# Optimization experiments

Measured on AMD Instinct MI355X. Metric: run time of the kernel, lower is better.

The kernel has to match this reference:

```python
import jax, jax.numpy as jnp
import numpy as np

DIM = 1024
DIM_HEAD = 64
HEADS = 8
MULT = 4
ATTN_INNER = HEADS * DIM_HEAD            # 512
FF_INNER = MULT * DIM                    # 4096
FUSED = ATTN_INNER + DIM_HEAD + DIM_HEAD + 2 * FF_INNER  # 8832


def setup_inputs() -> dict:
    key = jax.random.key(0)
    ks = jax.random.split(key, 5)
    x = jax.random.normal(ks[0], (2, 2048, DIM), dtype=jnp.float32)
    gamma = jnp.ones((DIM,), dtype=jnp.float32)
    # Linear weights stored as [in, out]
    w_fused = jax.random.normal(ks[1], (DIM, FUSED), dtype=jnp.float32) * (DIM ** -0.5)
    w_attn_out = jax.random.normal(ks[2], (ATTN_INNER, DIM), dtype=jnp.float32) * (ATTN_INNER ** -0.5)
    w_ff_out = jax.random.normal(ks[3], (FF_INNER, DIM), dtype=jnp.float32) * (FF_INNER ** -0.5)
    return {"x": x, "gamma": gamma, "w_fused": w_fused,
            "w_attn_out": w_attn_out, "w_ff_out": w_ff_out}


def _forward(x, gamma, w_fused, w_attn_out, w_ff_out):
    b, n, d = x.shape
    # LayerNorm (beta buffer is zeros)
    mu = jnp.mean(x, axis=-1, keepdims=True)
    var = jnp.mean(jnp.square(x - mu), axis=-1, keepdims=True)
    xn = (x - mu) * jax.lax.rsqrt(var + 1e-5) * gamma
    # fused QKV + FF projection
    proj = jnp.einsum('bnd,df->bnf', xn, w_fused)
    q = proj[..., :ATTN_INNER]
    k = proj[..., ATTN_INNER:ATTN_INNER + DIM_HEAD]
    v = proj[..., ATTN_INNER + DIM_HEAD:ATTN_INNER + 2 * DIM_HEAD]
    ff = proj[..., ATTN_INNER + 2 * DIM_HEAD:]
    # multi-query attention: single shared K/V head of width DIM_HEAD
    q = q.reshape(b, n, HEADS, DIM_HEAD).transpose(0, 2, 1, 3) * (DIM_HEAD ** -0.5)
    sim = jnp.einsum('bhid,bjd->bhij', q, k)
    attn = jax.nn.softmax(sim, axis=-1)
    out = jnp.einsum('bhij,bjd->bhid', attn, v)
    out = out.transpose(0, 2, 1, 3).reshape(b, n, ATTN_INNER)
    attn_out = jnp.einsum('bna,ad->bnd', out, w_attn_out)
    # parallel SwiGLU FF: chunk -> (x_part, gate); silu(gate)*x_part
    ff_x, gate = ff[..., :FF_INNER], ff[..., FF_INNER:]
    ff_out = jnp.einsum('bnf,fd->bnd', jax.nn.silu(gate) * ff_x, w_ff_out)
    return attn_out + ff_out


def reference(x, gamma, w_fused, w_attn_out, w_ff_out):
    return _forward(x, gamma, w_fused, w_attn_out, w_ff_out)
```

## Files before the change

### kernel.cpp

```cpp
#include <hip/hip_runtime.h>
#include <hip/hip_bf16.h>
#include <stdint.h>

#define DIM     1024
#define SEQ     2048
#define NTOK    4096
#define HEADS   8
#define DH      64
#define AINNER  512
#define FFI     4096
#define FUSED   8832
#define HCOLS   4608

typedef __attribute__((ext_vector_type(8))) short short8;
typedef __attribute__((ext_vector_type(4))) short short4v;
typedef __attribute__((ext_vector_type(4))) float f32x4;

__device__ __forceinline__ short f2bf(float f) {
  union { float f; uint32_t u; } v; v.f = f;
  uint32_t r = v.u + 0x7fffu + ((v.u >> 16) & 1u);
  return (short)(r >> 16);
}
__device__ __forceinline__ float bf2f(short s) {
  union { uint32_t u; float f; } v; v.u = ((uint32_t)(uint16_t)s) << 16;
  return v.f;
}
__device__ __forceinline__ void g2l16(const void* g, void* l) {
  __builtin_amdgcn_global_load_lds((const __attribute__((address_space(1))) void*)g,
                                   (__attribute__((address_space(3))) void*)l, 16, 0, 0);
}

#define PH_W4 asm volatile("s_waitcnt vmcnt(4)\ns_barrier" ::: "memory")
#define PH_W2 asm volatile("s_waitcnt vmcnt(2)\ns_barrier" ::: "memory")
#define PH_W0 asm volatile("s_waitcnt vmcnt(0)\ns_barrier" ::: "memory")
#define PH_B  asm volatile("s_barrier" ::: "memory")

__global__ __launch_bounds__(256) void k_prep(const float* __restrict__ wf,
                                              const float* __restrict__ wao,
                                              const float* __restrict__ wfo,
                                              const float* __restrict__ x,
                                              const float* __restrict__ gamma,
                                              short* __restrict__ WtF,
                                              short* __restrict__ Wt2,
                                              short* __restrict__ xn) {
  __shared__ short tile[32][33];
  __shared__ float red[8];
  int bid = blockIdx.x;
  if (bid < 8832) {
    int bx = bid % 276, by = bid / 276;
    int c0 = bx * 32, r0 = by * 32;
    int tx = threadIdx.x & 31, ty = threadIdx.x >> 5;
#pragma unroll
    for (int i = 0; i < 32; i += 8)
      tile[ty + i][tx] = f2bf(wf[(size_t)(r0 + ty + i) * FUSED + c0 + tx]);
    __syncthreads();
#pragma unroll
    for (int i = 0; i < 32; i += 8)
      WtF[(size_t)(c0 + ty + i) * DIM + r0 + tx] = tile[tx][ty + i];
  } else if (bid < 13440) {
    int idx = bid - 8832;
    int bx = idx & 31, by = idx >> 5;
    int c0 = bx * 32, r0 = by * 32;
    int tx = threadIdx.x & 31, ty = threadIdx.x >> 5;
#pragma unroll
    for (int i = 0; i < 32; i += 8) {
      int r = r0 + ty + i;
      float v = (r < AINNER) ? wao[(size_t)r * DIM + c0 + tx]
                             : wfo[(size_t)(r - AINNER) * DIM + c0 + tx];
      tile[ty + i][tx] = f2bf(v);
    }
    __syncthreads();
#pragma unroll
    for (int i = 0; i < 32; i += 8)
      Wt2[(size_t)(c0 + ty + i) * HCOLS + r0 + tx] = tile[tx][ty + i];
  } else {
    int row = bid - 13440;
    int t = threadIdx.x;
    const float4* xr = (const float4*)(x + (size_t)row * DIM);
    float4 v = xr[t];
    float s = v.x + v.y + v.z + v.w;
    float s2 = v.x * v.x + v.y * v.y + v.z * v.z + v.w * v.w;
#pragma unroll
    for (int m = 1; m < 64; m <<= 1) { s += __shfl_xor(s, m); s2 += __shfl_xor(s2, m); }
    int w = t >> 6;
    if ((t & 63) == 0) { red[w] = s; red[4 + w] = s2; }
    __syncthreads();
    s = red[0] + red[1] + red[2] + red[3];
    s2 = red[4] + red[5] + red[6] + red[7];
    float mu = s * (1.f / DIM);
    float rs = rsqrtf(s2 * (1.f / DIM) - mu * mu + 1e-5f);
    const float4* g4 = (const float4*)gamma;
    float4 g = g4[t];
    short4v o;
    o.x = f2bf((v.x - mu) * rs * g.x);
    o.y = f2bf((v.y - mu) * rs * g.y);
    o.z = f2bf((v.z - mu) * rs * g.z);
    o.w = f2bf((v.w - mu) * rs * g.w);
    ((short4v*)(xn + (size_t)row * DIM))[t] = o;
  }
}

__global__ __launch_bounds__(512, 2) void p1(const short* __restrict__ A,
                                             const short* __restrict__ Bt,
                                             short* __restrict__ qb,
                                             short* __restrict__ kbf,
                                             short* __restrict__ vtb,
                                             short* __restrict__ H) {
  extern __shared__ __align__(16) short S[];
  int tid = threadIdx.x, l = tid & 63, w = tid >> 6;
  int hw = blockIdx.y * 37 + blockIdx.x;
  int tile = (hw & 7) * 74 + (hw >> 3);
  int c = tile / 74, j = tile % 74;
  bool fused = j < 64;
  int bx, by;
  if (fused) { int f = c * 64 + j; by = f >> 5; bx = f & 31; }
  else       { int q = c * 10 + (j - 64); by = q / 5; bx = 32 + q % 5; }
  int mBase = by * 256;
  int b0row = fused ? (640 + bx * 128) : ((bx - 32) * 128);
  int b1row = 4736 + bx * 128;

  int srow = w * 8 + (l >> 3);
  int cs = (l & 7) ^ (l >> 3);
  const short* Ag = A + (size_t)(mBase + srow) * DIM + cs * 8;
  const short* Bg0 = Bt + (size_t)(b0row + srow) * DIM + cs * 8;
  const short* Bg1 = Bt + (size_t)(b1row + srow) * DIM + cs * 8;
  int dsto = w * 512 + l * 8;

#define STG_A0(kt, db) { _Pragma("unroll") for (int i = 0; i < 2; ++i) \
    g2l16(Ag + (size_t)(i * 64) * DIM + (kt) * 64, S + (db) * 16384 + i * 4096 + dsto); }
#define STG_A1(kt, db) { _Pragma("unroll") for (int i = 2; i < 4; ++i) \
    g2l16(Ag + (size_t)(i * 64) * DIM + (kt) * 64, S + (db) * 16384 + i * 4096 + dsto); }
#define STG_B0(kt, db) { _Pragma("unroll") for (int i = 0; i < 2; ++i) \
    g2l16(Bg0 + (size_t)(i * 64) * DIM + (kt) * 64, S + 32768 + (db) * 16384 + i * 4096 + dsto); }
#define STG_B1(kt, db) { _Pragma("unroll") for (int i = 0; i < 2; ++i) \
    g2l16(Bg1 + (size_t)(i * 64) * DIM + (kt) * 64, S + 32768 + (db) * 16384 + 8192 + i * 4096 + dsto); }

  const int NT = DIM / 64;
  int c0 = l & 15, kg = l >> 4, cx = l & 7;
  int ch0 = (kg ^ cx) * 8, ch1 = ((4 + kg) ^ cx) * 8;
  int r0 = (l >> 4) * 4;
  f32x4 zero = {0.f, 0.f, 0.f, 0.f};

  if (!fused) {
    STG_A0(0, 0); STG_A1(0, 0); STG_B0(0, 0);
    int wm = w >> 2, wn = w & 3;
    f32x4 acc[8][2];
#pragma unroll
    for (int m = 0; m < 8; ++m) { acc[m][0] = zero; acc[m][1] = zero; }
    for (int kt = 0; kt < NT; ++kt) {
      int db = kt & 1, dbn = db ^ 1;
      PH_W0;
      if (kt + 1 < NT) { STG_A0(kt + 1, dbn); STG_A1(kt + 1, dbn); STG_B0(kt + 1, dbn); }
      const short* Ab = S + db * 16384;
      const short* Bb = S + 32768 + db * 16384;
#pragma unroll
      for (int kkh = 0; kkh < 2; ++kkh) {
        int ch8 = kkh ? ch1 : ch0;
        short8 b0 = *(const short8*)(Bb + (wn * 32 + c0) * 64 + ch8);
        short8 b1 = *(const short8*)(Bb + (wn * 32 + 16 + c0) * 64 + ch8);
        __builtin_amdgcn_s_setprio(1);
#pragma unroll
        for (int m = 0; m < 8; ++m) {
          short8 a = *(const short8*)(Ab + (wm * 128 + m * 16 + c0) * 64 + ch8);
          acc[m][0] = __builtin_amdgcn_mfma_f32_16x16x32_bf16(a, b0, acc[m][0], 0, 0, 0);
          acc[m][1] = __builtin_amdgcn_mfma_f32_16x16x32_bf16(a, b1, acc[m][1], 0, 0, 0);
        }
        __builtin_amdgcn_s_setprio(0);
      }
    }
#pragma unroll
    for (int m = 0; m < 8; ++m)
#pragma unroll
      for (int n = 0; n < 2; ++n)
#pragma unroll
        for (int r = 0; r < 4; ++r) {
          float val = acc[m][n][r];
          int row = mBase + wm * 128 + m * 16 + r0 + r;
          int col = (bx - 32) * 128 + wn * 32 + n * 16 + c0;
          if (col < AINNER)
            qb[(size_t)row * AINNER + col] = f2bf(val);
          else if (col < AINNER + DH)
            kbf[(size_t)row * DH + (col - AINNER)] = f2bf(val);
          else
            vtb[((size_t)(row >> 11) * DH + (col - AINNER - DH)) * SEQ +
                (row & (SEQ - 1))] = f2bf(val);
        }
    return;
  }

  STG_A0(0, 0); STG_B0(0, 0); STG_B1(0, 0); STG_A1(0, 0);
  int ra = (w >> 2) * 64, rb = (w & 3) * 32;
  f32x4 acc[2][2][4][2];
#pragma unroll
  for (int a = 0; a < 2; ++a)
#pragma unroll
    for (int b = 0; b < 2; ++b)
#pragma unroll
      for (int m = 0; m < 4; ++m)
#pragma unroll
        for (int n = 0; n < 2; ++n) acc[a][b][m][n] = zero;

  for (int kt = 0; kt < NT; ++kt) {
    int db = kt & 1, dbn = db ^ 1;
    bool st = kt + 1 < NT;
    const short* Ab = S + db * 16384;
    const short* Bb = S + 32768 + db * 16384;
    short8 a1[4][2], a2[4][2], bF[2][2], bG[2][2];
    PH_W4;
#pragma unroll
    for (int m = 0; m < 4; ++m) {
      a1[m][0] = *(const short8*)(Ab + (ra + m * 16 + c0) * 64 + ch0);
      a1[m][1] = *(const short8*)(Ab + (ra + m * 16 + c0) * 64 + ch1);
    }
#pragma unroll
    for (int n = 0; n < 2; ++n) {
      bF[n][0] = *(const short8*)(Bb + (rb + n * 16 + c0) * 64 + ch0);
      bF[n][1] = *(const short8*)(Bb + (rb + n * 16 + c0) * 64 + ch1);
    }
    if (st) STG_A0(kt + 1, dbn);
    PH_B;
    __builtin_amdgcn_s_setprio(1);
#pragma unroll
    for (int m = 0; m < 4; ++m)
#pragma unroll
      for (int n = 0; n < 2; ++n) {
        acc[0][0][m][n] = __builtin_amdgcn_mfma_f32_16x16x32_bf16(a1[m][0], bF[n][0], acc[0][0][m][n], 0, 0, 0);
        acc[0][0][m][n] = __builtin_amdgcn_mfma_f32_16x16x32_bf16(a1[m][1], bF[n][1], acc[0][0][m][n], 0, 0, 0);
      }
    __builtin_amdgcn_s_setprio(0);
    if (st) PH_W4; else PH_W2;
#pragma unroll
    for (int n = 0; n < 2; ++n) {
      bG[n][0] = *(const short8*)(Bb + 8192 + (rb + n * 16 + c0) * 64 + ch0);
      bG[n][1] = *(const short8*)(Bb + 8192 + (rb + n * 16 + c0) * 64 + ch1);
    }
    if (st) STG_B0(kt + 1, dbn);
    PH_B;
    __builtin_amdgcn_s_setprio(1);
#pragma unroll
    for (int m = 0; m < 4; ++m)
#pragma unroll
      for (int n = 0; n < 2; ++n) {
        acc[0][1][m][n] = __builtin_amdgcn_mfma_f32_16x16x32_bf16(a1[m][0], bG[n][0], acc[0][1][m][n], 0, 0, 0);
        acc[0][1][m][n] = __builtin_amdgcn_mfma_f32_16x16x32_bf16(a1[m][1], bG[n][1], acc[0][1][m][n], 0, 0, 0);
      }
    __builtin_amdgcn_s_setprio(0);
    if (st) PH_W4; else PH_W0;
#pragma unroll
    for (int m = 0; m < 4; ++m) {
      a2[m][0] = *(const short8*)(Ab + 8192 + (ra + m * 16 + c0) * 64 + ch0);
      a2[m][1] = *(const short8*)(Ab + 8192 + (ra + m * 16 + c0) * 64 + ch1);
    }
    if (st) STG_B1(kt + 1, dbn);
    PH_B;
    __builtin_amdgcn_s_setprio(1);
#pragma unroll
    for (int m = 0; m < 4; ++m)
#pragma unroll
      for (int n = 0; n < 2; ++n) {
        acc[1][1][m][n] = __builtin_amdgcn_mfma_f32_16x16x32_bf16(a2[m][0], bG[n][0], acc[1][1][m][n], 0, 0, 0);
        acc[1][1][m][n] = __builtin_amdgcn_mfma_f32_16x16x32_bf16(a2[m][1], bG[n][1], acc[1][1][m][n], 0, 0, 0);
      }
    __builtin_amdgcn_s_setprio(0);
    if (st) STG_A1(kt + 1, dbn);
    __builtin_amdgcn_s_setprio(1);
#pragma unroll
    for (int m = 0; m < 4; ++m)
#pragma unroll
      for (int n = 0; n < 2; ++n) {
        acc[1][0][m][n] = __builtin_amdgcn_mfma_f32_16x16x32_bf16(a2[m][0], bF[n][0], acc[1][0][m][n], 0, 0, 0);
        acc[1][0][m][n] = __builtin_amdgcn_mfma_f32_16x16x32_bf16(a2[m][1], bF[n][1], acc[1][0][m][n], 0, 0, 0);
      }
    __builtin_amdgcn_s_setprio(0);
  }
#undef STG_A0
#undef STG_A1
#undef STG_B0
#undef STG_B1

#pragma unroll
  for (int a = 0; a < 2; ++a)
#pragma unroll
    for (int m = 0; m < 4; ++m)
#pragma unroll
      for (int n = 0; n < 2; ++n)
#pragma unroll
        for (int r = 0; r < 4; ++r) {
          int row = mBase + a * 128 + ra + m * 16 + r0 + r;
          int col = bx * 128 + rb + n * 16 + c0;
          float g = acc[a][1][m][n][r];
          float sg = g / (1.f + __expf(-g));
          H[(size_t)row * HCOLS + AINNER + col] = f2bf(sg * acc[a][0][m][n][r]);
        }
}

__global__ __launch_bounds__(512, 2) void gemm_s(const short* __restrict__ A,
                                                 const short* __restrict__ Bt,
                                                 short* __restrict__ part) {
  extern __shared__ __align__(16) short S[];
  int tid = threadIdx.x, l = tid & 63, w = tid >> 6;
  int hw = (blockIdx.z * 16 + blockIdx.y) * 4 + blockIdx.x;
  int tile = (hw & 7) * 32 + (hw >> 3);
  int bx = tile & 3, by = (tile >> 2) & 15, bz = tile >> 6;
  int mBase = by * 256, nBase = bx * 256;
  int kOff = bz * 1152;

  int srow = w * 8 + (l >> 3);
  int cs = (l & 7) ^ (l >> 3);
  const short* Ag = A + (size_t)(mBase + srow) * HCOLS + kOff + cs * 8;
  const short* Bg = Bt + (size_t)(nBase + srow) * HCOLS + kOff + cs * 8;
  int dsto = w * 512 + l * 8;

#define SG_A0(kt, db) { _Pragma("unroll") for (int i = 0; i < 2; ++i) \
    g2l16(Ag + (size_t)(i * 64) * HCOLS + (kt) * 64, S + (db) * 16384 + i * 4096 + dsto); }
#define SG_A1(kt, db) { _Pragma("unroll") for (int i = 2; i < 4; ++i) \
    g2l16(Ag + (size_t)(i * 64) * HCOLS + (kt) * 64, S + (db) * 16384 + i * 4096 + dsto); }
#define SG_B0(kt, db) { _Pragma("unroll") for (int i = 0; i < 2; ++i) \
    g2l16(Bg + (size_t)(i * 64) * HCOLS + (kt) * 64, S + 32768 + (db) * 16384 + i * 4096 + dsto); }
#define SG_B1(kt, db) { _Pragma("unroll") for (int i = 2; i < 4; ++i) \
    g2l16(Bg + (size_t)(i * 64) * HCOLS + (kt) * 64, S + 32768 + (db) * 16384 + i * 4096 + dsto); }

  const int NT = 18;
  SG_A0(0, 0); SG_B0(0, 0); SG_B1(0, 0); SG_A1(0, 0);

  int c0 = l & 15, kg = l >> 4, cx = l & 7;
  int ch0 = (kg ^ cx) * 8, ch1 = ((4 + kg) ^ cx) * 8;
  int ra = (w >> 2) * 64, rb = (w & 3) * 32;
  f32x4 zero = {0.f, 0.f, 0.f, 0.f};
  f32x4 acc[2][2][4][2];
#pragma unroll
  for (int a = 0; a < 2; ++a)
#pragma unroll
    for (int b = 0; b < 2; ++b)
#pragma unroll
      for (int m = 0; m < 4; ++m)
#pragma unroll
        for (int n = 0; n < 2; ++n) acc[a][b][m][n] = zero;

  for (int kt = 0; kt < NT; ++kt) {
    int db = kt & 1, dbn = db ^ 1;
    bool st = kt + 1 < NT;
    const short* Ab = S + db * 16384;
    const short* Bb = S + 32768 + db * 16384;
    short8 a1[4][2], a2[4][2], bF[2][2], bG[2][2];
    PH_W4;
#pragma unroll
    for (int m = 0; m < 4; ++m) {
      a1[m][0] = *(const short8*)(Ab + (ra + m * 16 + c0) * 64 + ch0);
      a1[m][1] = *(const short8*)(Ab + (ra + m * 16 + c0) * 64 + ch1);
    }
#pragma unroll
    for (int n = 0; n < 2; ++n) {
      bF[n][0] = *(const short8*)(Bb + (rb + n * 16 + c0) * 64 + ch0);
      bF[n][1] = *(const short8*)(Bb + (rb + n * 16 + c0) * 64 + ch1);
    }
    if (st) SG_A0(kt + 1, dbn);
    PH_B;
    __builtin_amdgcn_s_setprio(1);
#pragma unroll
    for (int m = 0; m < 4; ++m)
#pragma unroll
      for (int n = 0; n < 2; ++n) {
        acc[0][0][m][n] = __builtin_amdgcn_mfma_f32_16x16x32_bf16(a1[m][0], bF[n][0], acc[0][0][m][n], 0, 0, 0);
        acc[0][0][m][n] = __builtin_amdgcn_mfma_f32_16x16x32_bf16(a1[m][1], bF[n][1], acc[0][0][m][n], 0, 0, 0);
      }
    __builtin_amdgcn_s_setprio(0);
    if (st) PH_W4; else PH_W2;
#pragma unroll
    for (int n = 0; n < 2; ++n) {
      bG[n][0] = *(const short8*)(Bb + 8192 + (rb + n * 16 + c0) * 64 + ch0);
      bG[n][1] = *(const short8*)(Bb + 8192 + (rb + n * 16 + c0) * 64 + ch1);
    }
    if (st) SG_B0(kt + 1, dbn);
    PH_B;
    __builtin_amdgcn_s_setprio(1);
#pragma unroll
    for (int m = 0; m < 4; ++m)
#pragma unroll
      for (int n = 0; n < 2; ++n) {
        acc[0][1][m][n] = __builtin_amdgcn_mfma_f32_16x16x32_bf16(a1[m][0], bG[n][0], acc[0][1][m][n], 0, 0, 0);
        acc[0][1][m][n] = __builtin_amdgcn_mfma_f32_16x16x32_bf16(a1[m][1], bG[n][1], acc[0][1][m][n], 0, 0, 0);
      }
    __builtin_amdgcn_s_setprio(0);
    if (st) PH_W4; else PH_W0;
#pragma unroll
    for (int m = 0; m < 4; ++m) {
      a2[m][0] = *(const short8*)(Ab + 8192 + (ra + m * 16 + c0) * 64 + ch0);
      a2[m][1] = *(const short8*)(Ab + 8192 + (ra + m * 16 + c0) * 64 + ch1);
    }
    if (st) SG_B1(kt + 1, dbn);
    PH_B;
    __builtin_amdgcn_s_setprio(1);
#pragma unroll
    for (int m = 0; m < 4; ++m)
#pragma unroll
      for (int n = 0; n < 2; ++n) {
        acc[1][1][m][n] = __builtin_amdgcn_mfma_f32_16x16x32_bf16(a2[m][0], bG[n][0], acc[1][1][m][n], 0, 0, 0);
        acc[1][1][m][n] = __builtin_amdgcn_mfma_f32_16x16x32_bf16(a2[m][1], bG[n][1], acc[1][1][m][n], 0, 0, 0);
      }
    __builtin_amdgcn_s_setprio(0);
    if (st) SG_A1(kt + 1, dbn);
    __builtin_amdgcn_s_setprio(1);
#pragma unroll
    for (int m = 0; m < 4; ++m)
#pragma unroll
      for (int n = 0; n < 2; ++n) {
        acc[1][0][m][n] = __builtin_amdgcn_mfma_f32_16x16x32_bf16(a2[m][0], bF[n][0], acc[1][0][m][n], 0, 0, 0);
        acc[1][0][m][n] = __builtin_amdgcn_mfma_f32_16x16x32_bf16(a2[m][1], bF[n][1], acc[1][0][m][n], 0, 0, 0);
      }
    __builtin_amdgcn_s_setprio(0);
  }
#undef SG_A0
#undef SG_A1
#undef SG_B0
#undef SG_B1

  int r0 = (l >> 4) * 4;
#pragma unroll
  for (int a = 0; a < 2; ++a)
#pragma unroll
    for (int b = 0; b < 2; ++b)
#pragma unroll
      for (int m = 0; m < 4; ++m)
#pragma unroll
        for (int n = 0; n < 2; ++n)
#pragma unroll
          for (int r = 0; r < 4; ++r) {
            int row = mBase + a * 128 + ra + m * 16 + r0 + r;
            int col = nBase + b * 128 + rb + n * 16 + c0;
            part[(size_t)bz * (NTOK * DIM) + (size_t)row * DIM + col] = f2bf(acc[a][b][m][n][r]);
          }
}

__global__ __launch_bounds__(256) void k_red(const short* __restrict__ part,
                                             float* __restrict__ out) {
  int i = (blockIdx.x * 256 + threadIdx.x) * 8;
  float s[8] = {0.f, 0.f, 0.f, 0.f, 0.f, 0.f, 0.f, 0.f};
#pragma unroll
  for (int ks = 0; ks < 4; ++ks) {
    short8 v = *(const short8*)(part + (size_t)ks * (NTOK * DIM) + i);
#pragma unroll
    for (int jj = 0; jj < 8; ++jj) s[jj] += bf2f(v[jj]);
  }
  float4 lo = {s[0], s[1], s[2], s[3]};
  float4 hi = {s[4], s[5], s[6], s[7]};
  *(float4*)(out + i) = lo;
  *(float4*)(out + i + 4) = hi;
}

__global__ __launch_bounds__(256) void k_attn(const short* __restrict__ qb,
                                              const short* __restrict__ kb,
                                              const short* __restrict__ vt,
                                              short* __restrict__ H) {
  __shared__ __align__(16) short Qs[64 * 64];
  __shared__ __align__(16) short Ks[128 * 64];
  __shared__ __align__(16) short Vs[64 * 128];
  __shared__ __align__(16) short Ps[4][16 * 128];
  int t = threadIdx.x, l = t & 63, w = t >> 6;
  int qt = blockIdx.x, bh = blockIdx.y;
  int b = bh >> 3, h = bh & 7;
  int q0 = qt * 64;

  int srow = w * 8 + (l >> 3);
  int schunk = (l & 7) ^ (l >> 3);
  {
    const short* Qg = qb + (size_t)(b * SEQ + q0 + srow) * AINNER + h * DH + schunk * 8;
    short* qs = Qs + w * 512 + l * 8;
#pragma unroll
    for (int i = 0; i < 2; ++i) g2l16(Qg + (size_t)(i * 32) * AINNER, qs + i * 2048);
  }
  const short* Kg = kb + (size_t)(b * SEQ + srow) * DH + schunk * 8;
  short* ksl = Ks + w * 512 + l * 8;
  int vrow = w * 4 + (l >> 4);
  int vchunk = (l & 15) ^ (vrow & 7);
  const short* Vg = vt + (size_t)b * DH * SEQ + (size_t)vrow * SEQ + vchunk * 8;
  short* vsl = Vs + w * 512 + l * 8;

#pragma unroll
  for (int i = 0; i < 4; ++i) {
    g2l16(Kg + (size_t)(i * 32) * DH, ksl + i * 2048);
    g2l16(Vg + (size_t)(i * 16) * SEQ, vsl + i * 2048);
  }

  float m_run[4], l_run[4];
  f32x4 zero = {0.f, 0.f, 0.f, 0.f};
  f32x4 Oacc[4];
#pragma unroll
  for (int r = 0; r < 4; ++r) { m_run[r] = -1e30f; l_run[r] = 0.f; }
#pragma unroll
  for (int n = 0; n < 4; ++n) Oacc[n] = zero;

  int c0 = l & 15, kg = l >> 4, cx = l & 7;
  short* pw = Ps[w];

  for (int kv0 = 0; kv0 < SEQ; kv0 += 128) {
    asm volatile("s_waitcnt vmcnt(0)\ns_barrier" ::: "memory");

    f32x4 sacc[8];
#pragma unroll
    for (int n = 0; n < 8; ++n) sacc[n] = zero;
#pragma unroll
    for (int kk = 0; kk < 2; ++kk) {
      int rr = w * 16 + c0;
      short8 aq = *(const short8*)(Qs + rr * 64 + ((kk * 4 + kg) ^ cx) * 8);
#pragma unroll
      for (int n = 0; n < 8; ++n) {
        int kr = n * 16 + c0;
        short8 bk = *(const short8*)(Ks + kr * 64 + ((kk * 4 + kg) ^ cx) * 8);
        sacc[n] = __builtin_amdgcn_mfma_f32_16x16x32_bf16(aq, bk, sacc[n], 0, 0, 0);
      }
    }
#pragma unroll
    for (int r = 0; r < 4; ++r) {
      float mx = -1e30f;
#pragma unroll
      for (int n = 0; n < 8; ++n) {
        sacc[n][r] *= 0.125f;
        mx = fmaxf(mx, sacc[n][r]);
      }
#pragma unroll
      for (int msk = 1; msk < 16; msk <<= 1) mx = fmaxf(mx, __shfl_xor(mx, msk));
      float nm = fmaxf(m_run[r], mx);
      float corr = __expf(m_run[r] - nm);
      m_run[r] = nm;
      float rs = 0.f;
#pragma unroll
      for (int n = 0; n < 8; ++n) {
        float p = __expf(sacc[n][r] - nm);
        sacc[n][r] = p;
        rs += p;
      }
#pragma unroll
      for (int msk = 1; msk < 16; msk <<= 1) rs += __shfl_xor(rs, msk);
      l_run[r] = l_run[r] * corr + rs;
      Oacc[0][r] *= corr; Oacc[1][r] *= corr; Oacc[2][r] *= corr; Oacc[3][r] *= corr;
    }
#pragma unroll
    for (int n = 0; n < 8; ++n)
#pragma unroll
      for (int r = 0; r < 4; ++r) {
        int pr = (l >> 4) * 4 + r;
        int pc = n * 16 + c0;
        pw[pr * 128 + ((pc >> 3) ^ (pr & 7)) * 8 + (pc & 7)] = f2bf(sacc[n][r]);
      }
    asm volatile("s_waitcnt lgkmcnt(0)" ::: "memory");
#pragma unroll
    for (int kk = 0; kk < 4; ++kk) {
      int pr = c0;
      short8 ap = *(const short8*)(pw + pr * 128 + ((kk * 4 + kg) ^ cx) * 8);
#pragma unroll
      for (int n = 0; n < 4; ++n) {
        int vr = n * 16 + c0;
        short8 bv = *(const short8*)(Vs + vr * 128 + ((kk * 4 + kg) ^ (vr & 7)) * 8);
        Oacc[n] = __builtin_amdgcn_mfma_f32_16x16x32_bf16(ap, bv, Oacc[n], 0, 0, 0);
      }
    }
    __syncthreads();
    int nx = kv0 + 128;
    if (nx < SEQ) {
#pragma unroll
      for (int i = 0; i < 4; ++i) {
        g2l16(Kg + (size_t)(nx + i * 32) * DH, ksl + i * 2048);
        g2l16(Vg + nx + (size_t)(i * 16) * SEQ, vsl + i * 2048);
      }
    }
  }
#pragma unroll
  for (int r = 0; r < 4; ++r) {
    float inv = 1.f / l_run[r];
    int row = b * SEQ + q0 + w * 16 + (l >> 4) * 4 + r;
#pragma unroll
    for (int n = 0; n < 4; ++n) {
      int col = h * DH + n * 16 + c0;
      H[(size_t)row * HCOLS + col] = f2bf(Oacc[n][r] * inv);
    }
  }
}

extern "C" void kernel_launch(void* const* d_in, const int* in_sizes, int n_in,
                              void* d_out, int out_size, void* d_ws, size_t ws_size,
                              hipStream_t stream) {
  const float* x     = (const float*)d_in[0];
  const float* gamma = (const float*)d_in[1];
  const float* w_f   = (const float*)d_in[2];
  const float* w_ao  = (const float*)d_in[3];
  const float* w_fo  = (const float*)d_in[4];
  float* out = (float*)d_out;

  char* ws = (char*)d_ws;
  size_t o = 0;
  short* WtF = (short*)(ws + o); o += (size_t)FUSED * DIM * 2;
  short* Wt2 = (short*)(ws + o); o += (size_t)DIM * HCOLS * 2;
  short* xn  = (short*)(ws + o); o += (size_t)NTOK * DIM * 2;
  short* qb  = (short*)(ws + o); o += (size_t)NTOK * AINNER * 2;
  short* kbf = (short*)(ws + o); o += (size_t)NTOK * DH * 2;
  short* vtb = (short*)(ws + o); o += (size_t)NTOK * DH * 2;
  short* H   = (short*)(ws + o); o += (size_t)NTOK * HCOLS * 2;
  short* part = (short*)(ws + o);

  k_prep<<<17536, 256, 0, stream>>>(w_f, w_ao, w_fo, x, gamma, WtF, Wt2, xn);
  p1<<<dim3(37, 16), 512, 131072, stream>>>(xn, WtF, qb, kbf, vtb, H);
  k_attn<<<dim3(32, 16), 256, 0, stream>>>(qb, kbf, vtb, H);
  gemm_s<<<dim3(4, 16, 4), 512, 131072, stream>>>(H, Wt2, part);
  k_red<<<NTOK * DIM / 2048, 256, 0, stream>>>(part, out);
}
```

Baseline: 207.3 us.

## Deepen GEMM global-to-LDS prefetch to two stages ahead with relaxed waits

Restructures the async global-to-LDS load schedule in both bf16 GEMM kernels so that quarter-tiles for k-step kt+2 are issued into the buffer just consumed, and only one quarter (A1) is loaded one step ahead. The vmcnt waits are relaxed to allow more loads in flight, and several barriers are removed, to hide global memory latency better. Final iterations reissue redundant loads instead of branching, which adds some extra memory traffic. The correctness of reusing a buffer while other waves may still read it depends on the remaining barriers.

```diff
diff --git a/kernel.cpp b/kernel.cpp
--- a/kernel.cpp
+++ b/kernel.cpp
@@ -30,8 +30,7 @@
                                    (__attribute__((address_space(3))) void*)l, 16, 0, 0);
 }
 
-#define PH_W4 asm volatile("s_waitcnt vmcnt(4)\ns_barrier" ::: "memory")
-#define PH_W2 asm volatile("s_waitcnt vmcnt(2)\ns_barrier" ::: "memory")
+#define PW10 asm volatile("s_waitcnt vmcnt(10)\ns_barrier" ::: "memory")
 #define PH_W0 asm volatile("s_waitcnt vmcnt(0)\ns_barrier" ::: "memory")
 #define PH_B  asm volatile("s_barrier" ::: "memory")
 
@@ -189,6 +188,7 @@
   }
 
   STG_A0(0, 0); STG_B0(0, 0); STG_B1(0, 0); STG_A1(0, 0);
+  STG_A0(1, 1); STG_B0(1, 1); STG_B1(1, 1);
   int ra = (w >> 2) * 64, rb = (w & 3) * 32;
   f32x4 acc[2][2][4][2];
 #pragma unroll
@@ -202,11 +202,12 @@
 
   for (int kt = 0; kt < NT; ++kt) {
     int db = kt & 1, dbn = db ^ 1;
-    bool st = kt + 1 < NT;
+    int tA1 = (kt + 1 < NT) ? kt + 1 : kt;
+    int tN  = (kt + 2 < NT) ? kt + 2 : kt;
     const short* Ab = S + db * 16384;
     const short* Bb = S + 32768 + db * 16384;
     short8 a1[4][2], a2[4][2], bF[2][2], bG[2][2];
-    PH_W4;
+    PW10;
 #pragma unroll
     for (int m = 0; m < 4; ++m) {
       a1[m][0] = *(const short8*)(Ab + (ra + m * 16 + c0) * 64 + ch0);
@@ -217,8 +218,7 @@
       bF[n][0] = *(const short8*)(Bb + (rb + n * 16 + c0) * 64 + ch0);
       bF[n][1] = *(const short8*)(Bb + (rb + n * 16 + c0) * 64 + ch1);
     }
-    if (st) STG_A0(kt + 1, dbn);
-    PH_B;
+    STG_A1(tA1, dbn);
     __builtin_amdgcn_s_setprio(1);
 #pragma unroll
     for (int m = 0; m < 4; ++m)
@@ -228,14 +228,13 @@
         acc[0][0][m][n] = __builtin_amdgcn_mfma_f32_16x16x32_bf16(a1[m][1], bF[n][1], acc[0][0][m][n], 0, 0, 0);
       }
     __builtin_amdgcn_s_setprio(0);
-    if (st) PH_W4; else PH_W2;
+    PW10;
 #pragma unroll
     for (int n = 0; n < 2; ++n) {
       bG[n][0] = *(const short8*)(Bb + 8192 + (rb + n * 16 + c0) * 64 + ch0);
       bG[n][1] = *(const short8*)(Bb + 8192 + (rb + n * 16 + c0) * 64 + ch1);
     }
-    if (st) STG_B0(kt + 1, dbn);
-    PH_B;
+    STG_A0(tN, db);
     __builtin_amdgcn_s_setprio(1);
 #pragma unroll
     for (int m = 0; m < 4; ++m)
@@ -245,14 +244,13 @@
         acc[0][1][m][n] = __builtin_amdgcn_mfma_f32_16x16x32_bf16(a1[m][1], bG[n][1], acc[0][1][m][n], 0, 0, 0);
       }
     __builtin_amdgcn_s_setprio(0);
-    if (st) PH_W4; else PH_W0;
+    PW10;
 #pragma unroll
     for (int m = 0; m < 4; ++m) {
       a2[m][0] = *(const short8*)(Ab + 8192 + (ra + m * 16 + c0) * 64 + ch0);
       a2[m][1] = *(const short8*)(Ab + 8192 + (ra + m * 16 + c0) * 64 + ch1);
     }
-    if (st) STG_B1(kt + 1, dbn);
-    PH_B;
+    STG_B0(tN, db);
     __builtin_amdgcn_s_setprio(1);
 #pragma unroll
     for (int m = 0; m < 4; ++m)
@@ -262,7 +260,8 @@
         acc[1][1][m][n] = __builtin_amdgcn_mfma_f32_16x16x32_bf16(a2[m][1], bG[n][1], acc[1][1][m][n], 0, 0, 0);
       }
     __builtin_amdgcn_s_setprio(0);
-    if (st) STG_A1(kt + 1, dbn);
+    PH_B;
+    STG_B1(tN, db);
     __builtin_amdgcn_s_setprio(1);
 #pragma unroll
     for (int m = 0; m < 4; ++m)
@@ -273,6 +272,7 @@
       }
     __builtin_amdgcn_s_setprio(0);
   }
+  asm volatile("s_waitcnt vmcnt(0)" ::: "memory");
 #undef STG_A0
 #undef STG_A1
 #undef STG_B0
@@ -322,6 +322,7 @@
 
   const int NT = 18;
   SG_A0(0, 0); SG_B0(0, 0); SG_B1(0, 0); SG_A1(0, 0);
+  SG_A0(1, 1); SG_B0(1, 1); SG_B1(1, 1);
 
   int c0 = l & 15, kg = l >> 4, cx = l & 7;
   int ch0 = (kg ^ cx) * 8, ch1 = ((4 + kg) ^ cx) * 8;
@@ -339,11 +340,12 @@
 
   for (int kt = 0; kt < NT; ++kt) {
     int db = kt & 1, dbn = db ^ 1;
-    bool st = kt + 1 < NT;
+    int tA1 = (kt + 1 < NT) ? kt + 1 : kt;
+    int tN  = (kt + 2 < NT) ? kt + 2 : kt;
     const short* Ab = S + db * 16384;
     const short* Bb = S + 32768 + db * 16384;
     short8 a1[4][2], a2[4][2], bF[2][2], bG[2][2];
-    PH_W4;
+    PW10;
 #pragma unroll
     for (int m = 0; m < 4; ++m) {
       a1[m][0] = *(const short8*)(Ab + (ra + m * 16 + c0) * 64 + ch0);
@@ -354,8 +356,7 @@
       bF[n][0] = *(const short8*)(Bb + (rb + n * 16 + c0) * 64 + ch0);
       bF[n][1] = *(const short8*)(Bb + (rb + n * 16 + c0) * 64 + ch1);
     }
-    if (st) SG_A0(kt + 1, dbn);
-    PH_B;
+    SG_A1(tA1, dbn);
     __builtin_amdgcn_s_setprio(1);
 #pragma unroll
     for (int m = 0; m < 4; ++m)
@@ -365,14 +366,13 @@
         acc[0][0][m][n] = __builtin_amdgcn_mfma_f32_16x16x32_bf16(a1[m][1], bF[n][1], acc[0][0][m][n], 0, 0, 0);
       }
     __builtin_amdgcn_s_setprio(0);
-    if (st) PH_W4; else PH_W2;
+    PW10;
 #pragma unroll
     for (int n = 0; n < 2; ++n) {
       bG[n][0] = *(const short8*)(Bb + 8192 + (rb + n * 16 + c0) * 64 + ch0);
       bG[n][1] = *(const short8*)(Bb + 8192 + (rb + n * 16 + c0) * 64 + ch1);
     }
-    if (st) SG_B0(kt + 1, dbn);
-    PH_B;
+    SG_A0(tN, db);
     __builtin_amdgcn_s_setprio(1);
 #pragma unroll
     for (int m = 0; m < 4; ++m)
@@ -382,14 +382,13 @@
         acc[0][1][m][n] = __builtin_amdgcn_mfma_f32_16x16x32_bf16(a1[m][1], bG[n][1], acc[0][1][m][n], 0, 0, 0);
       }
     __builtin_amdgcn_s_setprio(0);
-    if (st) PH_W4; else PH_W0;
+    PW10;
 #pragma unroll
     for (int m = 0; m < 4; ++m) {
       a2[m][0] = *(const short8*)(Ab + 8192 + (ra + m * 16 + c0) * 64 + ch0);
       a2[m][1] = *(const short8*)(Ab + 8192 + (ra + m * 16 + c0) * 64 + ch1);
     }
-    if (st) SG_B1(kt + 1, dbn);
-    PH_B;
+    SG_B0(tN, db);
     __builtin_amdgcn_s_setprio(1);
 #pragma unroll
     for (int m = 0; m < 4; ++m)
@@ -399,7 +398,8 @@
         acc[1][1][m][n] = __builtin_amdgcn_mfma_f32_16x16x32_bf16(a2[m][1], bG[n][1], acc[1][1][m][n], 0, 0, 0);
       }
     __builtin_amdgcn_s_setprio(0);
-    if (st) SG_A1(kt + 1, dbn);
+    PH_B;
+    SG_B1(tN, db);
     __builtin_amdgcn_s_setprio(1);
 #pragma unroll
     for (int m = 0; m < 4; ++m)
@@ -410,6 +410,7 @@
       }
     __builtin_amdgcn_s_setprio(0);
   }
+  asm volatile("s_waitcnt vmcnt(0)" ::: "memory");
 #undef SG_A0
 #undef SG_A1
 #undef SG_B0
```

Result: no change. 210.2 us (+1.4%).
